# Kernel tuning notes

Hardware: AMD Instinct MI355X
Metric: run time of the kernel (lower is better)

The kernel has to match this reference:

```python
import math
import jax, jax.numpy as jnp
import numpy as np

SCALE = 64.0
MARGIN = 0.5
EPS = 1e-07
COS_M = math.cos(MARGIN)
SIN_M = math.sin(MARGIN)
TH = math.cos(math.pi - MARGIN)
MM = math.sin(math.pi - MARGIN) * MARGIN

N, D, C = 512, 512, 100000


def setup_inputs() -> dict:
    key = jax.random.key(0)
    k1, k2, k3 = jax.random.split(key, 3)
    input = jax.random.normal(k1, (N, D), dtype=jnp.float32)
    weight = jax.random.normal(k2, (C, D), dtype=jnp.float32)
    target = jax.random.randint(k3, (N,), 0, C, dtype=jnp.int64)
    return {"input": input, "target": target, "weight": weight}


def _l2_normalize(x, axis=-1, eps=1e-12):
    # matches F.normalize: x / max(||x||, eps)
    n = jnp.linalg.norm(x, axis=axis, keepdims=True)
    return x / jnp.maximum(n, eps)


def reference(input, target, weight):
    x = _l2_normalize(input)            # [N, D]
    w = _l2_normalize(weight)           # [C, D]
    cosine = jnp.clip(jnp.einsum('nd,cd->nc', x, w), -1.0 + EPS, 1.0 - EPS)  # [N, C]
    sine = jnp.sqrt(jnp.clip(1.0 - cosine * cosine, -1.0 + EPS, 1.0 - EPS))
    phi = cosine * COS_M - sine * SIN_M
    # easy_margin=False branch
    phi = jnp.where(cosine > TH, phi, cosine - MM)
    one_hot = jax.nn.one_hot(target, C, dtype=jnp.bool_)  # [N, C]
    logits = jnp.where(one_hot, phi, cosine) * SCALE
    # cross entropy (mean reduction)
    logp = jax.nn.log_softmax(logits, axis=-1)
    nll = -jnp.take_along_axis(logp, target[:, None], axis=1)[:, 0]
    return jnp.mean(nll)
```

## Files before the change

### kernel.cpp

```cpp
#include <hip/hip_runtime.h>
#include <hip/hip_bf16.h>
#include <math.h>
#include <stdint.h>

#define N_S 512
#define D_S 512
#define C_S 100000
#define SCALEF 64.0f
#define EPSV 1e-7f
#define COS_M 0.8775825618903728f
#define SIN_M 0.4794255386042030f
#define TH_C (-0.8775825618903728f)
#define MM_C 0.2397127693021015f

#define BM 128
#define BC 128
#define BK 64
#define NCB ((C_S + BC - 1) / BC)
#define PPR (NCB * 2)
#define NWG (4 * NCB)
#define CHUNK (NWG / 8)

typedef __attribute__((ext_vector_type(8))) short bf16x8;
typedef __attribute__((ext_vector_type(4))) float f32x4;

#define GLOAD_LDS16(g, l)                                                     \
    __builtin_amdgcn_global_load_lds(                                         \
        (const __attribute__((address_space(1))) unsigned int*)(g),           \
        (__attribute__((address_space(3))) unsigned int*)(l), 16, 0, 0)

__device__ __forceinline__ short f2bf(float f) {
    uint32_t u = __builtin_bit_cast(uint32_t, f);
    u += 0x7FFFu + ((u >> 16) & 1u);
    return (short)(u >> 16);
}

__global__ void xnorm_k(const float* __restrict__ x, short* __restrict__ xb) {
    int row = blockIdx.x;
    int tid = threadIdx.x;
    float2 v = *(const float2*)(x + (size_t)row * D_S + tid * 2);
    float ss = v.x * v.x + v.y * v.y;
    #pragma unroll
    for (int m = 1; m < 64; m <<= 1) ss += __shfl_xor(ss, m);
    __shared__ float sred[4];
    if ((tid & 63) == 0) sred[tid >> 6] = ss;
    __syncthreads();
    float tot = sred[0] + sred[1] + sred[2] + sred[3];
    float scale = 1.0f / fmaxf(sqrtf(tot), 1e-12f);
    short2 o;
    o.x = f2bf(v.x * scale);
    o.y = f2bf(v.y * scale);
    *(short2*)(xb + (size_t)row * D_S + tid * 2) = o;
}

__global__ void wnc_k(const float* __restrict__ w, short* __restrict__ wb) {
    int c = blockIdx.x * 4 + (threadIdx.x >> 6);
    int lane = threadIdx.x & 63;
    const float4* p = (const float4*)(w + (size_t)c * D_S);
    float4 a = p[lane];
    float4 b = p[lane + 64];
    float ss = a.x * a.x + a.y * a.y + a.z * a.z + a.w * a.w
             + b.x * b.x + b.y * b.y + b.z * b.z + b.w * b.w;
    #pragma unroll
    for (int m = 1; m < 64; m <<= 1) ss += __shfl_xor(ss, m);
    float sc = 1.0f / fmaxf(sqrtf(ss), 1e-12f);
    short4 o1, o2;
    o1.x = f2bf(a.x * sc); o1.y = f2bf(a.y * sc);
    o1.z = f2bf(a.z * sc); o1.w = f2bf(a.w * sc);
    o2.x = f2bf(b.x * sc); o2.y = f2bf(b.y * sc);
    o2.z = f2bf(b.z * sc); o2.w = f2bf(b.w * sc);
    *(short4*)(wb + (size_t)c * D_S + lane * 4) = o1;
    *(short4*)(wb + (size_t)c * D_S + 256 + lane * 4) = o2;
}

__global__ void wnorm_k(const float* __restrict__ w, float* __restrict__ winv) {
    int c = blockIdx.x * 4 + (threadIdx.x >> 6);
    int lane = threadIdx.x & 63;
    const float4* p = (const float4*)(w + (size_t)c * D_S);
    float4 a = p[lane];
    float4 b = p[lane + 64];
    float ss = a.x * a.x + a.y * a.y + a.z * a.z + a.w * a.w
             + b.x * b.x + b.y * b.y + b.z * b.z + b.w * b.w;
    #pragma unroll
    for (int m = 1; m < 64; m <<= 1) ss += __shfl_xor(ss, m);
    if (lane == 0) winv[c] = 1.0f / fmaxf(sqrtf(ss), 1e-12f);
}

__device__ __forceinline__ void arc_epilogue(f32x4 acc[4][4], const int* tgts,
                                             int row0, int col0, int cb,
                                             int wm, int wn, int lane,
                                             float* partM, float* partS,
                                             float* tgtlogit) {
    int lg  = lane >> 4;
    int l15 = lane & 15;
    #pragma unroll
    for (int mr = 0; mr < 4; mr++) {
        #pragma unroll
        for (int r = 0; r < 4; r++) {
            int row_l = wm * 64 + mr * 16 + lg * 4 + r;
            int row_g = row0 + row_l;
            int tg = tgts[row_l];
            float lv[4];
            #pragma unroll
            for (int nc = 0; nc < 4; nc++) {
                int c_g = col0 + wn * 64 + nc * 16 + l15;
                float cosv = acc[mr][nc][r];
                cosv = fminf(fmaxf(cosv, -1.0f + EPSV), 1.0f - EPSV);
                float lo = cosv * SCALEF;
                if (c_g == tg) {
                    float s2 = 1.0f - cosv * cosv;
                    s2 = fminf(fmaxf(s2, -1.0f + EPSV), 1.0f - EPSV);
                    float sine = sqrtf(s2);
                    float phi = cosv * COS_M - sine * SIN_M;
                    if (!(cosv > TH_C)) phi = cosv - MM_C;
                    lo = phi * SCALEF;
                    tgtlogit[row_g] = lo;
                }
                if (c_g >= C_S) lo = -INFINITY;
                lv[nc] = lo;
            }
            float m = fmaxf(fmaxf(lv[0], lv[1]), fmaxf(lv[2], lv[3]));
            #pragma unroll
            for (int d = 1; d < 16; d <<= 1) m = fmaxf(m, __shfl_xor(m, d));
            float s = 0.0f;
            #pragma unroll
            for (int nc = 0; nc < 4; nc++)
                if (lv[nc] > -INFINITY) s += __expf(lv[nc] - m);
            #pragma unroll
            for (int d = 1; d < 16; d <<= 1) s += __shfl_xor(s, d);
            if (l15 == 0) {
                int pi = row_g * PPR + cb * 2 + wn;
                partM[pi] = m;
                partS[pi] = s;
            }
        }
    }
}

__global__ void gemm2_k(const short* __restrict__ xb,
                        const short* __restrict__ wb,
                        const int* __restrict__ tgt,
                        float* __restrict__ partM,
                        float* __restrict__ partS,
                        float* __restrict__ tgtlogit) {
    __shared__ short Alds[BM * BK];
    __shared__ short Blds[BC * BK];
    __shared__ int tgts[BM];

    int orig = blockIdx.x;
    int swz  = (orig & 7) * CHUNK + (orig >> 3);
    int rb = swz & 3, cb = swz >> 2;
    int row0 = rb * BM, col0 = cb * BC;
    int tid = threadIdx.x, wid = tid >> 6, lane = tid & 63;
    int wm = wid >> 1, wn = wid & 1;

    if (tid < BM) tgts[tid] = tgt[row0 + tid];

    f32x4 acc[4][4] = {};

    int lr    = lane >> 3;
    int kslot = (lane & 7) ^ lr;
    const short* aS[4];
    const short* bS[4];
    #pragma unroll
    for (int p = 0; p < 4; p++) {
        int rloc = (p * 4 + wid) * 8 + lr;
        aS[p] = xb + (size_t)(row0 + rloc) * D_S + kslot * 8;
        int cg = col0 + rloc;
        if (cg >= C_S) cg = C_S - 1;
        bS[p] = wb + (size_t)cg * D_S + kslot * 8;
    }

    int l15 = lane & 15, lg = lane >> 4;

    for (int kt = 0; kt < D_S; kt += BK) {
        __syncthreads();
        #pragma unroll
        for (int p = 0; p < 4; p++) {
            GLOAD_LDS16(aS[p] + kt, (char*)Alds + (p * 4 + wid) * 1024);
            GLOAD_LDS16(bS[p] + kt, (char*)Blds + (p * 4 + wid) * 1024);
        }
        __syncthreads();
        #pragma unroll
        for (int kk = 0; kk < BK; kk += 32) {
            int slot = (kk >> 3) + lg;
            bf16x8 af[4], bfr[4];
            #pragma unroll
            for (int mr = 0; mr < 4; mr++) {
                int r = wm * 64 + mr * 16 + l15;
                af[mr] = *(const bf16x8*)((char*)Alds + r * 128 +
                                          ((slot ^ (r & 7)) << 4));
            }
            #pragma unroll
            for (int nc = 0; nc < 4; nc++) {
                int c = wn * 64 + nc * 16 + l15;
                bfr[nc] = *(const bf16x8*)((char*)Blds + c * 128 +
                                           ((slot ^ (c & 7)) << 4));
            }
            #pragma unroll
            for (int mr = 0; mr < 4; mr++)
                #pragma unroll
                for (int nc = 0; nc < 4; nc++)
                    acc[mr][nc] = __builtin_amdgcn_mfma_f32_16x16x32_bf16(
                        af[mr], bfr[nc], acc[mr][nc], 0, 0, 0);
        }
    }

    arc_epilogue(acc, tgts, row0, col0, cb, wm, wn, lane, partM, partS, tgtlogit);
}

__global__ void gemm_arc_k(const short* __restrict__ xb,
                           const float* __restrict__ w,
                           const float* __restrict__ winv,
                           const int* __restrict__ tgt,
                           float* __restrict__ partM,
                           float* __restrict__ partS,
                           float* __restrict__ tgtlogit) {
    __shared__ short Alds[BM * BK];
    __shared__ short Blds[BC * BK];
    __shared__ int tgts[BM];

    int rb = blockIdx.x;
    int cb = blockIdx.y;
    int row0 = rb * BM;
    int col0 = cb * BC;
    int tid = threadIdx.x;
    int wid = tid >> 6;
    int lane = tid & 63;
    int wm = wid >> 1;
    int wn = wid & 1;

    if (tid < BM) tgts[tid] = tgt[row0 + tid];

    f32x4 acc[4][4] = {};

    int bc_r = tid >> 1;
    int bkh  = (tid & 1) * 32;
    int cg   = col0 + bc_r;
    int csrc = cg < C_S ? cg : C_S - 1;
    float wi = winv[csrc];

    for (int kt = 0; kt < D_S; kt += BK) {
        __syncthreads();
        #pragma unroll
        for (int p = 0; p < 4; p++) {
            int flat = p * 4096 + tid * 16;
            int m  = flat >> 7;
            int kb = (flat & 127) >> 1;
            *(int4*)((char*)Alds + flat) =
                *(const int4*)(xb + (size_t)(row0 + m) * D_S + kt + kb);
        }
        {
            const float4* wp = (const float4*)(w + (size_t)csrc * D_S + kt + bkh);
            char* bdst = (char*)Blds + bc_r * 128 + bkh * 2;
            #pragma unroll
            for (int j = 0; j < 8; j++) {
                float4 v = wp[j];
                short4 o;
                o.x = f2bf(v.x * wi);
                o.y = f2bf(v.y * wi);
                o.z = f2bf(v.z * wi);
                o.w = f2bf(v.w * wi);
                *(short4*)(bdst + j * 8) = o;
            }
        }
        __syncthreads();
        #pragma unroll
        for (int kk = 0; kk < BK; kk += 32) {
            int krow = kk + ((lane >> 4) << 3);
            bf16x8 af[4], bfr[4];
            #pragma unroll
            for (int mr = 0; mr < 4; mr++) {
                int r = wm * 64 + mr * 16 + (lane & 15);
                af[mr] = *(const bf16x8*)((char*)Alds + r * 128 + krow * 2);
            }
            #pragma unroll
            for (int nc = 0; nc < 4; nc++) {
                int c = wn * 64 + nc * 16 + (lane & 15);
                bfr[nc] = *(const bf16x8*)((char*)Blds + c * 128 + krow * 2);
            }
            #pragma unroll
            for (int mr = 0; mr < 4; mr++)
                #pragma unroll
                for (int nc = 0; nc < 4; nc++)
                    acc[mr][nc] = __builtin_amdgcn_mfma_f32_16x16x32_bf16(
                        af[mr], bfr[nc], acc[mr][nc], 0, 0, 0);
        }
    }

    arc_epilogue(acc, tgts, row0, col0, cb, wm, wn, lane, partM, partS, tgtlogit);
}

__global__ void reduce_k(const float* __restrict__ partM,
                         const float* __restrict__ partS,
                         const float* __restrict__ tgtlogit,
                         float* __restrict__ nll) {
    int row = blockIdx.x;
    int tid = threadIdx.x;
    float m = -INFINITY, s = 0.0f;
    for (int p = tid; p < PPR; p += 256) {
        float mp = partM[(size_t)row * PPR + p];
        float sp = partS[(size_t)row * PPR + p];
        if (sp > 0.0f) {
            float mn = fmaxf(m, mp);
            s = s * __expf(m - mn) + sp * __expf(mp - mn);
            m = mn;
        }
    }
    __shared__ float rm[256], rs[256];
    rm[tid] = m; rs[tid] = s;
    __syncthreads();
    for (int h = 128; h > 0; h >>= 1) {
        if (tid < h) {
            float mp = rm[tid + h], sp = rs[tid + h];
            if (sp > 0.0f) {
                float mn = fmaxf(rm[tid], mp);
                rs[tid] = rs[tid] * __expf(rm[tid] - mn) + sp * __expf(mp - mn);
                rm[tid] = mn;
            }
        }
        __syncthreads();
    }
    if (tid == 0) nll[row] = (rm[0] + logf(rs[0])) - tgtlogit[row];
}

__global__ void finalize_k(const float* __restrict__ nll, float* __restrict__ out) {
    int tid = threadIdx.x;
    float v = nll[tid] + nll[tid + 256];
    #pragma unroll
    for (int d = 1; d < 64; d <<= 1) v += __shfl_xor(v, d);
    __shared__ float sr[4];
    if ((tid & 63) == 0) sr[tid >> 6] = v;
    __syncthreads();
    if (tid == 0) out[0] = (sr[0] + sr[1] + sr[2] + sr[3]) * (1.0f / 512.0f);
}

extern "C" void kernel_launch(void* const* d_in, const int* in_sizes, int n_in,
                              void* d_out, int out_size, void* d_ws, size_t ws_size,
                              hipStream_t stream) {
    const float* x   = (const float*)d_in[0];
    const int*   tgt = (const int*)d_in[1];
    const float* w   = (const float*)d_in[2];
    float* out = (float*)d_out;
    char* ws = (char*)d_ws;

    short* xb  = (short*)(ws + 0);
    float* tgl = (float*)(ws + 524288);
    float* nll = (float*)(ws + 526336);
    float* pM  = (float*)(ws + 528384);
    float* pS  = (float*)(ws + 3731456);
    short* wb  = (short*)(ws + 6934528);

    if (ws_size >= 109334528ULL) {
        xnorm_k<<<512, 256, 0, stream>>>(x, xb);
        wnc_k<<<C_S / 4, 256, 0, stream>>>(w, wb);
        gemm2_k<<<NWG, 256, 0, stream>>>(xb, wb, tgt, pM, pS, tgl);
        reduce_k<<<512, 256, 0, stream>>>(pM, pS, tgl, nll);
        finalize_k<<<1, 256, 0, stream>>>(nll, out);
    } else {
        float* winv = (float*)(ws + 524288);
        float* tglf = (float*)(ws + 924288);
        float* nllf = (float*)(ws + 926336);
        float* pMf  = (float*)(ws + 928384);
        float* pSf  = (float*)(ws + 4131456);
        xnorm_k<<<512, 256, 0, stream>>>(x, xb);
        wnorm_k<<<C_S / 4, 256, 0, stream>>>(w, winv);
        dim3 g(4, NCB);
        gemm_arc_k<<<g, 256, 0, stream>>>(xb, w, winv, tgt, pMf, pSf, tglf);
        reduce_k<<<512, 256, 0, stream>>>(pMf, pSf, tglf, nllf);
        finalize_k<<<1, 256, 0, stream>>>(nllf, out);
    }
}
```

Before: 394.5 us.

## Double-buffer LDS with BK=32 and prefetch next tile during MFMA

Rewrites the main GEMM kernel to use two LDS buffers with a K-step of 32. The next tile's global-to-LDS loads are issued before computing on the current tile, so there is one barrier per step instead of two. A new XOR swizzle is used for the 64-byte rows, and launch bounds request 4 blocks per SM. The aim is to hide global load latency behind MFMA work, at the cost of more loop iterations and barrier overhead per K.

```diff
diff --git a/kernel.cpp b/kernel.cpp
--- a/kernel.cpp
+++ b/kernel.cpp
@@ -15,7 +15,7 @@
 
 #define BM 128
 #define BC 128
-#define BK 64
+#define BK2 32
 #define NCB ((C_S + BC - 1) / BC)
 #define PPR (NCB * 2)
 #define NWG (4 * NCB)
@@ -137,14 +137,15 @@
     }
 }
 
-__global__ void gemm2_k(const short* __restrict__ xb,
-                        const short* __restrict__ wb,
-                        const int* __restrict__ tgt,
-                        float* __restrict__ partM,
-                        float* __restrict__ partS,
-                        float* __restrict__ tgtlogit) {
-    __shared__ short Alds[BM * BK];
-    __shared__ short Blds[BC * BK];
+__global__ void __launch_bounds__(256, 4)
+gemm3_k(const short* __restrict__ xb,
+        const short* __restrict__ wb,
+        const int* __restrict__ tgt,
+        float* __restrict__ partM,
+        float* __restrict__ partS,
+        float* __restrict__ tgtlogit) {
+    __shared__ short Alds[2][BM * BK2];
+    __shared__ short Blds[2][BC * BK2];
     __shared__ int tgts[BM];
 
     int orig = blockIdx.x;
@@ -153,57 +154,83 @@
     int row0 = rb * BM, col0 = cb * BC;
     int tid = threadIdx.x, wid = tid >> 6, lane = tid & 63;
     int wm = wid >> 1, wn = wid & 1;
+    int l15 = lane & 15, lg = lane >> 4;
 
     if (tid < BM) tgts[tid] = tgt[row0 + tid];
 
     f32x4 acc[4][4] = {};
 
-    int lr    = lane >> 3;
-    int kslot = (lane & 7) ^ lr;
-    const short* aS[4];
-    const short* bS[4];
-    #pragma unroll
-    for (int p = 0; p < 4; p++) {
-        int rloc = (p * 4 + wid) * 8 + lr;
+    int sub   = tid >> 2;
+    int kslot = (tid & 3) ^ (sub & 3) ^ ((sub >> 2) & 3);
+    const short* aS[2];
+    const short* bS[2];
+    #pragma unroll
+    for (int p = 0; p < 2; p++) {
+        int rloc = p * 64 + sub;
         aS[p] = xb + (size_t)(row0 + rloc) * D_S + kslot * 8;
         int cg = col0 + rloc;
         if (cg >= C_S) cg = C_S - 1;
         bS[p] = wb + (size_t)cg * D_S + kslot * 8;
     }
 
-    int l15 = lane & 15, lg = lane >> 4;
-
-    for (int kt = 0; kt < D_S; kt += BK) {
+    #pragma unroll
+    for (int p = 0; p < 2; p++) {
+        GLOAD_LDS16(aS[p], (char*)Alds[0] + p * 4096 + wid * 1024);
+        GLOAD_LDS16(bS[p], (char*)Blds[0] + p * 4096 + wid * 1024);
+    }
+    __syncthreads();
+
+    int cur = 0;
+    #pragma unroll 1
+    for (int step = 0; step < 15; ++step) {
+        int ktn = (step + 1) * BK2;
+        #pragma unroll
+        for (int p = 0; p < 2; p++) {
+            GLOAD_LDS16(aS[p] + ktn, (char*)Alds[cur ^ 1] + p * 4096 + wid * 1024);
+            GLOAD_LDS16(bS[p] + ktn, (char*)Blds[cur ^ 1] + p * 4096 + wid * 1024);
+        }
+        bf16x8 af[4], bfr[4];
+        #pragma unroll
+        for (int mr = 0; mr < 4; mr++) {
+            int r = wm * 64 + mr * 16 + l15;
+            int phys = lg ^ (r & 3) ^ ((r >> 2) & 3);
+            af[mr] = *(const bf16x8*)((char*)Alds[cur] + r * 64 + (phys << 4));
+        }
+        #pragma unroll
+        for (int nc = 0; nc < 4; nc++) {
+            int c = wn * 64 + nc * 16 + l15;
+            int phys = lg ^ (c & 3) ^ ((c >> 2) & 3);
+            bfr[nc] = *(const bf16x8*)((char*)Blds[cur] + c * 64 + (phys << 4));
+        }
+        #pragma unroll
+        for (int mr = 0; mr < 4; mr++)
+            #pragma unroll
+            for (int nc = 0; nc < 4; nc++)
+                acc[mr][nc] = __builtin_amdgcn_mfma_f32_16x16x32_bf16(
+                    af[mr], bfr[nc], acc[mr][nc], 0, 0, 0);
         __syncthreads();
-        #pragma unroll
-        for (int p = 0; p < 4; p++) {
-            GLOAD_LDS16(aS[p] + kt, (char*)Alds + (p * 4 + wid) * 1024);
-            GLOAD_LDS16(bS[p] + kt, (char*)Blds + (p * 4 + wid) * 1024);
-        }
-        __syncthreads();
-        #pragma unroll
-        for (int kk = 0; kk < BK; kk += 32) {
-            int slot = (kk >> 3) + lg;
-            bf16x8 af[4], bfr[4];
-            #pragma unroll
-            for (int mr = 0; mr < 4; mr++) {
-                int r = wm * 64 + mr * 16 + l15;
-                af[mr] = *(const bf16x8*)((char*)Alds + r * 128 +
-                                          ((slot ^ (r & 7)) << 4));
-            }
-            #pragma unroll
-            for (int nc = 0; nc < 4; nc++) {
-                int c = wn * 64 + nc * 16 + l15;
-                bfr[nc] = *(const bf16x8*)((char*)Blds + c * 128 +
-                                           ((slot ^ (c & 7)) << 4));
-            }
-            #pragma unroll
-            for (int mr = 0; mr < 4; mr++)
-                #pragma unroll
-                for (int nc = 0; nc < 4; nc++)
-                    acc[mr][nc] = __builtin_amdgcn_mfma_f32_16x16x32_bf16(
-                        af[mr], bfr[nc], acc[mr][nc], 0, 0, 0);
-        }
+        cur ^= 1;
+    }
+    {
+        bf16x8 af[4], bfr[4];
+        #pragma unroll
+        for (int mr = 0; mr < 4; mr++) {
+            int r = wm * 64 + mr * 16 + l15;
+            int phys = lg ^ (r & 3) ^ ((r >> 2) & 3);
+            af[mr] = *(const bf16x8*)((char*)Alds[cur] + r * 64 + (phys << 4));
+        }
+        #pragma unroll
+        for (int nc = 0; nc < 4; nc++) {
+            int c = wn * 64 + nc * 16 + l15;
+            int phys = lg ^ (c & 3) ^ ((c >> 2) & 3);
+            bfr[nc] = *(const bf16x8*)((char*)Blds[cur] + c * 64 + (phys << 4));
+        }
+        #pragma unroll
+        for (int mr = 0; mr < 4; mr++)
+            #pragma unroll
+            for (int nc = 0; nc < 4; nc++)
+                acc[mr][nc] = __builtin_amdgcn_mfma_f32_16x16x32_bf16(
+                    af[mr], bfr[nc], acc[mr][nc], 0, 0, 0);
     }
 
     arc_epilogue(acc, tgts, row0, col0, cb, wm, wn, lane, partM, partS, tgtlogit);
@@ -216,8 +243,8 @@
                            float* __restrict__ partM,
                            float* __restrict__ partS,
                            float* __restrict__ tgtlogit) {
-    __shared__ short Alds[BM * BK];
-    __shared__ short Blds[BC * BK];
+    __shared__ short Alds[BM * 64];
+    __shared__ short Blds[BC * 64];
     __shared__ int tgts[BM];
 
     int rb = blockIdx.x;
@@ -240,7 +267,7 @@
     int csrc = cg < C_S ? cg : C_S - 1;
     float wi = winv[csrc];
 
-    for (int kt = 0; kt < D_S; kt += BK) {
+    for (int kt = 0; kt < D_S; kt += 64) {
         __syncthreads();
         #pragma unroll
         for (int p = 0; p < 4; p++) {
@@ -266,7 +293,7 @@
         }
         __syncthreads();
         #pragma unroll
-        for (int kk = 0; kk < BK; kk += 32) {
+        for (int kk = 0; kk < 64; kk += 32) {
             int krow = kk + ((lane >> 4) << 3);
             bf16x8 af[4], bfr[4];
             #pragma unroll
@@ -354,7 +381,7 @@
     if (ws_size >= 109334528ULL) {
         xnorm_k<<<512, 256, 0, stream>>>(x, xb);
         wnc_k<<<C_S / 4, 256, 0, stream>>>(w, wb);
-        gemm2_k<<<NWG, 256, 0, stream>>>(xb, wb, tgt, pM, pS, tgl);
+        gemm3_k<<<NWG, 256, 0, stream>>>(xb, wb, tgt, pM, pS, tgl);
         reduce_k<<<512, 256, 0, stream>>>(pM, pS, tgl, nll);
         finalize_k<<<1, 256, 0, stream>>>(nll, out);
     } else {
```

Result: slower. 402.9 us (+2.1%).
